# Kernel optimization log

Hardware: AMD Instinct MI355X
Metric: run time of the kernel (lower is better)

## Reference

```python
import jax, jax.numpy as jnp
import numpy as np

HIDDEN = 2048
HEADS = 16
HEAD_DIM = HIDDEN // HEADS  # 128
B, S = 2, 2048
SCALE = 1.0 / np.sqrt(HEAD_DIM)


def setup_inputs() -> dict:
    key = jax.random.key(0)
    ks = jax.random.split(key, 9)
    x = jax.random.normal(ks[0], (B, S, HIDDEN), dtype=jnp.float32)
    # causal mask, broadcastable to [B, 1(group), H, S, S]
    mask = jnp.tril(jnp.ones((S, S), dtype=bool))[None, None, None, :, :]
    mask = jnp.broadcast_to(mask, (B, 1, 1, S, S))
    s = 0.02
    Wq = jax.random.normal(ks[1], (HIDDEN, HIDDEN), dtype=jnp.float32) * s
    bq = jnp.zeros((HIDDEN,), dtype=jnp.float32)
    Wk = jax.random.normal(ks[2], (HIDDEN, HEAD_DIM), dtype=jnp.float32) * s
    bk = jnp.zeros((HEAD_DIM,), dtype=jnp.float32)
    Wv = jax.random.normal(ks[3], (HIDDEN, HEAD_DIM), dtype=jnp.float32) * s
    bv = jnp.zeros((HEAD_DIM,), dtype=jnp.float32)
    Wo = jax.random.normal(ks[4], (HIDDEN, HIDDEN), dtype=jnp.float32) * s
    bo = jnp.zeros((HIDDEN,), dtype=jnp.float32)
    return {"x": x, "mask": mask, "Wq": Wq, "bq": bq, "Wk": Wk, "bk": bk,
            "Wv": Wv, "bv": bv, "Wo": Wo, "bo": bo}


def reference(x, mask, Wq, bq, Wk, bk, Wv, bv, Wo, bo):
    b, s, _ = x.shape
    q = (x @ Wq + bq).reshape(b, s, HEADS, HEAD_DIM)   # [b,s,h,d]
    k = x @ Wk + bk                                    # [b,t,d] single shared KV head
    v = x @ Wv + bv                                    # [b,t,d]
    # scores: [b, h, s, t]; add group dim to match mask [b,1,h,s,t]
    scores = jnp.einsum('bshd,btd->bhst', q, k) * SCALE
    scores = scores[:, None]                            # [b,1,h,s,t]
    scores = jnp.where(mask, scores, jnp.float32(-jnp.inf))
    att = jax.nn.softmax(scores, axis=-1)[:, 0]         # [b,h,s,t] (dropout eval = identity)
    out = jnp.einsum('bhst,btd->bshd', att, v).reshape(b, s, HIDDEN)
    return out @ Wo + bo
```

## Files before the change

kernel.cpp:

```cpp
#include <hip/hip_runtime.h>


#define HIDDEN 2048
#define NHEADS 16
#define HDIM 128
#define BATCH 2
#define SEQ 2048
#define SCALE_L2E 0.1275258653864023f

typedef __attribute__((ext_vector_type(8))) short bfrag;
typedef __attribute__((ext_vector_type(4))) float facc;
typedef __attribute__((ext_vector_type(4))) unsigned int uifrag;

__device__ __forceinline__ unsigned short f2bf(float f) {
  unsigned int u = __float_as_uint(f);
  u += 0x7fffu + ((u >> 16) & 1u);
  return (unsigned short)(u >> 16);
}

__device__ __forceinline__ unsigned int cvt_pk_bf16(float lo, float hi) {
  unsigned int r;
  asm("v_cvt_pk_bf16_f32 %0, %1, %2" : "=v"(r) : "v"(lo), "v"(hi));
  return r;
}

__device__ __forceinline__ void gl_lds16(const void* g, void* l) {
  __builtin_amdgcn_global_load_lds(
      (const __attribute__((address_space(1))) void*)g,
      (__attribute__((address_space(3))) void*)l, 16, 0, 0);
}

#define SBAR() __builtin_amdgcn_s_barrier()
#define CFENCE() asm volatile("" ::: "memory")
#define WAIT_VM(n) asm volatile("s_waitcnt vmcnt(" #n ")" ::: "memory")

__global__ __launch_bounds__(256) void prep(const float* __restrict__ x,
                                            unsigned int* __restrict__ xb4,
                                            const float* __restrict__ Wq,
                                            const float* __restrict__ Wk,
                                            const float* __restrict__ Wv,
                                            const float* __restrict__ Wo,
                                            short* __restrict__ WqkvT,
                                            short* __restrict__ WoT, int n4) {
  if (blockIdx.z == 2) {
    int stride = gridDim.x * gridDim.y * 256;
    int i = ((int)blockIdx.y * gridDim.x + blockIdx.x) * 256 + threadIdx.x;
    for (; i < n4; i += stride) {
      float4 v = ((const float4*)x)[i];
      uint2 o = {cvt_pk_bf16(v.x, v.y), cvt_pk_bf16(v.z, v.w)};
      ((uint2*)xb4)[i] = o;
    }
    return;
  }
  const float* W;
  short* WT;
  int N;
  float s;
  int bx = blockIdx.x;
  if (blockIdx.z == 0) {
    if (bx < 64) { W = Wq; WT = WqkvT; N = HIDDEN; s = SCALE_L2E; }
    else { W = Wk; WT = WqkvT + (size_t)HIDDEN * HIDDEN; N = HDIM; s = 1.f; bx -= 64; }
  } else {
    if (bx < 64) { W = Wo; WT = WoT; N = HIDDEN; s = 1.f; }
    else { W = Wv; WT = WqkvT + (size_t)(HIDDEN + HDIM) * HIDDEN; N = HDIM; s = 1.f; bx -= 64; }
  }
  __shared__ float t[32][33];
  int tx = threadIdx.x & 31, ty = threadIdx.x >> 5;
  int n0 = bx * 32, k0 = blockIdx.y * 32;
#pragma unroll
  for (int j = 0; j < 4; ++j)
    t[ty + j * 8][tx] = W[(size_t)(k0 + ty + j * 8) * N + n0 + tx];
  __syncthreads();
#pragma unroll
  for (int j = 0; j < 4; ++j)
    WT[(size_t)(n0 + ty + j * 8) * HIDDEN + k0 + tx] = (short)f2bf(t[tx][ty + j * 8] * s);
}

__device__ __forceinline__ int pv_perm64(int row) {
  int k = row & 63;
  int p = (k & 0x23) | ((k & 0x0C) << 1) | ((k & 0x10) >> 2);
  return (row & ~63) | p;
}

__global__ __launch_bounds__(512, 6) void gemm_qkv(const short* __restrict__ A,
                                                   const short* __restrict__ BT,
                                                   const float* __restrict__ bq,
                                                   const float* __restrict__ bk,
                                                   const float* __restrict__ bv,
                                                   unsigned short* __restrict__ Qb,
                                                   unsigned short* __restrict__ Kb,
                                                   unsigned short* __restrict__ Vtb,
                                                   int M, int K) {
  __shared__ __align__(16) short Al[2][128 * 32];
  __shared__ __align__(16) short Bl[2][128 * 32];
  const int tid = threadIdx.x;
  const int w = tid >> 6, l = tid & 63;
  const int wm = w >> 1, wn = w & 1;
  const int l15 = l & 15, l4 = l >> 4;
  const int m0 = blockIdx.x * 128, n0 = blockIdx.y * 128;

  const short *ap, *bp;
  {
    int C = w * 64 + l;
    int row = C >> 2, c = C & 3;
    int sz = (c ^ (row & 3)) << 3;
    ap = A + (size_t)(m0 + row) * K + sz;
    bp = BT + (size_t)(n0 + row) * K + sz;
  }
  int aoffs[2], boffs[4];
#pragma unroll
  for (int mt = 0; mt < 2; ++mt) {
    int row = wm * 32 + mt * 16 + l15;
    aoffs[mt] = row * 64 + ((l4 ^ (row & 3)) << 4);
  }
#pragma unroll
  for (int nt = 0; nt < 4; ++nt) {
    int row = wn * 64 + nt * 16 + l15;
    boffs[nt] = row * 64 + ((l4 ^ (row & 3)) << 4);
  }

  facc acc[2][4] = {};
  const int nkt = K >> 5;
  gl_lds16(ap, &Al[0][w * 512]);
  gl_lds16(bp, &Bl[0][w * 512]);
  for (int kt = 0; kt < nkt; ++kt) {
    const int cur = kt & 1;
    if (kt + 1 < nkt) {
      gl_lds16(ap + (kt + 1) * 32, &Al[cur ^ 1][w * 512]);
      gl_lds16(bp + (kt + 1) * 32, &Bl[cur ^ 1][w * 512]);
      WAIT_VM(2);
    } else {
      WAIT_VM(0);
    }
    SBAR();
    CFENCE();
    const char* AlB = (const char*)Al + (cur << 13);
    const char* BlB = (const char*)Bl + (cur << 13);
    __builtin_amdgcn_s_setprio(1);
    bfrag af[2], bf[4];
#pragma unroll
    for (int mt = 0; mt < 2; ++mt) af[mt] = *(const bfrag*)(AlB + aoffs[mt]);
#pragma unroll
    for (int nt = 0; nt < 4; ++nt) bf[nt] = *(const bfrag*)(BlB + boffs[nt]);
#pragma unroll
    for (int mt = 0; mt < 2; ++mt)
#pragma unroll
      for (int nt = 0; nt < 4; ++nt)
        acc[mt][nt] = __builtin_amdgcn_mfma_f32_16x16x32_bf16(af[mt], bf[nt],
                                                              acc[mt][nt], 0, 0, 0);
    __builtin_amdgcn_s_setprio(0);
    CFENCE();
    SBAR();
    CFENCE();
  }
#pragma unroll
  for (int mt = 0; mt < 2; ++mt) {
#pragma unroll
    for (int nt = 0; nt < 4; ++nt) {
#pragma unroll
      for (int r = 0; r < 4; ++r) {
        int row = m0 + wm * 32 + mt * 16 + l4 * 4 + r;
        int col = n0 + wn * 64 + nt * 16 + l15;
        float v = acc[mt][nt][r];
        if (col < HIDDEN) {
          Qb[(size_t)row * HIDDEN + col] = f2bf(v + bq[col] * SCALE_L2E);
        } else if (col < HIDDEN + HDIM) {
          int lc = col - HIDDEN;
          Kb[(size_t)row * HDIM + lc] = f2bf(v + bk[lc]);
        } else {
          int lc = col - HIDDEN - HDIM;
          Vtb[(size_t)lc * M + pv_perm64(row)] = f2bf(v + bv[lc]);
        }
      }
    }
  }
}

#define GEMM_STAGE8(buf, kt)                                                   \
  _Pragma("unroll") for (int it_ = 0; it_ < 2; ++it_) {                        \
    gl_lds16(ap[it_] + (kt) * 64, &Al[buf][(w * 2 + it_) * 512]);              \
    gl_lds16(bp[it_] + (kt) * 64, &Bl[buf][(w * 2 + it_) * 512]);              \
  }

__global__ __launch_bounds__(512, 4) void gemm_out(const short* __restrict__ A,
                                                   const short* __restrict__ BT,
                                                   const float* __restrict__ bias,
                                                   float* __restrict__ Cout,
                                                   int M, int N, int K) {
  __shared__ __align__(16) short Al[2][128 * 64];
  __shared__ __align__(16) short Bl[2][128 * 64];
  const int tid = threadIdx.x;
  const int w = tid >> 6, l = tid & 63;
  const int wm = w >> 1, wn = w & 1;
  const int l15 = l & 15, l4 = l >> 4;
  const int m0 = blockIdx.x * 128, n0 = blockIdx.y * 128;
  facc acc[2][4] = {};
  const int nkt = K >> 6;
  const short *ap[2], *bp[2];
#pragma unroll
  for (int it_ = 0; it_ < 2; ++it_) {
    int C = (w * 2 + it_) * 64 + l;
    int row = C >> 3, c = C & 7;
    int sz = (c ^ (row & 7)) << 3;
    ap[it_] = A + (size_t)(m0 + row) * K + sz;
    bp[it_] = BT + (size_t)(n0 + row) * K + sz;
  }
  int aoffs[2][2], boffs[2][4];
#pragma unroll
  for (int ks = 0; ks < 2; ++ks) {
#pragma unroll
    for (int mt = 0; mt < 2; ++mt) {
      int row = wm * 32 + mt * 16 + l15, c = ks * 4 + l4;
      aoffs[ks][mt] = row * 128 + ((c ^ (row & 7)) << 4);
    }
#pragma unroll
    for (int nt = 0; nt < 4; ++nt) {
      int row = wn * 64 + nt * 16 + l15, c = ks * 4 + l4;
      boffs[ks][nt] = row * 128 + ((c ^ (row & 7)) << 4);
    }
  }
  GEMM_STAGE8(0, 0)
  for (int kt = 0; kt < nkt; ++kt) {
    const int cur = kt & 1;
    if (kt + 1 < nkt) {
      GEMM_STAGE8(cur ^ 1, kt + 1)
      WAIT_VM(4);
    } else {
      WAIT_VM(0);
    }
    SBAR();
    CFENCE();
    const char* AlB = (const char*)Al + (cur << 14);
    const char* BlB = (const char*)Bl + (cur << 14);
    __builtin_amdgcn_s_setprio(1);
#pragma unroll
    for (int ks = 0; ks < 2; ++ks) {
      bfrag af[2], bf[4];
#pragma unroll
      for (int mt = 0; mt < 2; ++mt) af[mt] = *(const bfrag*)(AlB + aoffs[ks][mt]);
#pragma unroll
      for (int nt = 0; nt < 4; ++nt) bf[nt] = *(const bfrag*)(BlB + boffs[ks][nt]);
#pragma unroll
      for (int mt = 0; mt < 2; ++mt)
#pragma unroll
        for (int nt = 0; nt < 4; ++nt)
          acc[mt][nt] = __builtin_amdgcn_mfma_f32_16x16x32_bf16(af[mt], bf[nt],
                                                                acc[mt][nt], 0, 0, 0);
    }
    __builtin_amdgcn_s_setprio(0);
    CFENCE();
    SBAR();
    CFENCE();
  }
#pragma unroll
  for (int mt = 0; mt < 2; ++mt)
#pragma unroll
    for (int nt = 0; nt < 4; ++nt)
#pragma unroll
      for (int r = 0; r < 4; ++r) {
        int row = m0 + wm * 32 + mt * 16 + l4 * 4 + r;
        int col = n0 + wn * 64 + nt * 16 + l15;
        Cout[(size_t)row * N + col] = acc[mt][nt][r] + bias[col];
      }
}

__global__ __launch_bounds__(256, 2) void attn_kernel(const short* __restrict__ Q,
                                                      const short* __restrict__ Kg,
                                                      const short* __restrict__ Vt,
                                                      unsigned short* __restrict__ O) {
  __shared__ __align__(16) short Kl[2][64 * 128];
  __shared__ __align__(16) short Vl[2][128 * 64];
  const int tid = threadIdx.x;
  const int w = tid >> 6, l = tid & 63;
  const int l15 = l & 15, l4 = l >> 4;
  const int h = blockIdx.y, b = blockIdx.z;

  int kgo[4], vgo[4];
#pragma unroll
  for (int it = 0; it < 4; ++it) {
    int C = (w * 4 + it) * 64 + l;
    int key = C >> 4, ck = C & 15;
    kgo[it] = key * HDIM + ((ck ^ (key & 7)) << 3);
    int d = C >> 3, cv = C & 7;
    vgo[it] = d * (BATCH * SEQ) + ((cv ^ (d & 7)) << 3);
  }
  int koffs[16], voffs[16];
#pragma unroll
  for (int kk = 0; kk < 4; ++kk)
#pragma unroll
    for (int kt = 0; kt < 4; ++kt) {
      int key = kt * 16 + l15, c = kk * 4 + l4;
      koffs[kk * 4 + kt] = key * 256 + ((c ^ (key & 7)) << 4);
    }
#pragma unroll
  for (int c = 0; c < 2; ++c)
#pragma unroll
    for (int nt = 0; nt < 8; ++nt) {
      int d = nt * 16 + l15, cc = c * 4 + l4;
      voffs[c * 8 + nt] = d * 128 + ((cc ^ (d & 7)) << 4);
    }
  const short* kg0 = Kg + (size_t)b * SEQ * HDIM;
  const short* vg0 = Vt + (size_t)b * SEQ;

#define STAGE_KV(buf, t)                                                       \
  do {                                                                         \
    const short* kgp = kg0 + (size_t)(t) * (64 * HDIM);                        \
    const short* vgp = vg0 + (size_t)(t) * 64;                                 \
    _Pragma("unroll") for (int it = 0; it < 4; ++it)                           \
        gl_lds16(kgp + kgo[it], &Kl[buf][(w * 4 + it) * 512]);                 \
    _Pragma("unroll") for (int it = 0; it < 4; ++it)                           \
        gl_lds16(vgp + vgo[it], &Vl[buf][(w * 4 + it) * 512]);                 \
  } while (0)

  for (int pass = 0; pass < 2; ++pass) {
    const int qtile = (pass == 0) ? (int)blockIdx.x : 31 - (int)blockIdx.x;
    const int q0 = qtile * 64;
    const int qw = q0 + w * 16;

    bfrag aq[4];
#pragma unroll
    for (int kk = 0; kk < 4; ++kk)
      aq[kk] = *(const bfrag*)(Q + (size_t)(b * SEQ + qw + l15) * HIDDEN +
                               h * HDIM + kk * 32 + l4 * 8);

    facc accO[8] = {};
    float mrow = -INFINITY, lrow = 0.f;
    const int nkv = qtile + 1;

    STAGE_KV(0, 0);

    for (int t = 0; t < nkv; ++t) {
      const int cur = t & 1;
      if (t + 1 < nkv) {
        STAGE_KV(cur ^ 1, t + 1);
        WAIT_VM(8);
      } else {
        WAIT_VM(0);
      }
      SBAR();
      CFENCE();
      const int kv0 = t << 6;
      const char* KlB = (const char*)Kl + (cur << 14);
      const char* VlB = (const char*)Vl + (cur << 14);

      facc sac[4] = {};
      __builtin_amdgcn_s_setprio(1);
#pragma unroll
      for (int kk = 0; kk < 4; ++kk) {
#pragma unroll
        for (int kt = 0; kt < 4; ++kt) {
          bfrag ak = *(const bfrag*)(KlB + koffs[kk * 4 + kt]);
          sac[kt] = __builtin_amdgcn_mfma_f32_16x16x32_bf16(ak, aq[kk], sac[kt], 0, 0, 0);
        }
      }
      __builtin_amdgcn_s_setprio(0);

      bfrag bv[16];
#pragma unroll
      for (int i = 0; i < 16; ++i)
        bv[i] = *(const bfrag*)(VlB + voffs[i]);
      CFENCE();
      SBAR();
      CFENCE();

      const int qg = qw + l15;
      const bool needmask = (kv0 + 63 > qw);
      float p[4][4];
#pragma unroll
      for (int kt = 0; kt < 4; ++kt)
#pragma unroll
        for (int r = 0; r < 4; ++r) {
          float v = sac[kt][r];
          if (needmask) {
            int keyg = kv0 + kt * 16 + l4 * 4 + r;
            v = (keyg <= qg) ? v : -INFINITY;
          }
          p[kt][r] = v;
        }
      float m0_ = fmaxf(fmaxf(p[0][0], p[0][1]), fmaxf(p[0][2], p[0][3]));
      float m1_ = fmaxf(fmaxf(p[1][0], p[1][1]), fmaxf(p[1][2], p[1][3]));
      float m2_ = fmaxf(fmaxf(p[2][0], p[2][1]), fmaxf(p[2][2], p[2][3]));
      float m3_ = fmaxf(fmaxf(p[3][0], p[3][1]), fmaxf(p[3][2], p[3][3]));
      float mt = fmaxf(fmaxf(m0_, m1_), fmaxf(m2_, m3_));
      mt = fmaxf(mt, __shfl_xor(mt, 16));
      mt = fmaxf(mt, __shfl_xor(mt, 32));
      if (!__all(mt <= mrow + 8.0f)) {
        float mn = fmaxf(mrow, mt);
        float f = exp2f(mrow - mn);
        mrow = mn;
        lrow *= f;
        float fr[4];
#pragma unroll
        for (int r = 0; r < 4; ++r) fr[r] = __shfl(f, l4 * 4 + r);
#pragma unroll
        for (int nt = 0; nt < 8; ++nt)
#pragma unroll
          for (int r = 0; r < 4; ++r) accO[nt][r] *= fr[r];
      }
#pragma unroll
      for (int kt = 0; kt < 4; ++kt)
#pragma unroll
        for (int r = 0; r < 4; ++r) p[kt][r] = exp2f(p[kt][r] - mrow);
      float s0_ = (p[0][0] + p[0][1]) + (p[0][2] + p[0][3]);
      float s1_ = (p[1][0] + p[1][1]) + (p[1][2] + p[1][3]);
      float s2_ = (p[2][0] + p[2][1]) + (p[2][2] + p[2][3]);
      float s3_ = (p[3][0] + p[3][1]) + (p[3][2] + p[3][3]);
      float ps = (s0_ + s1_) + (s2_ + s3_);
      ps += __shfl_xor(ps, 16);
      ps += __shfl_xor(ps, 32);
      lrow += ps;

      __builtin_amdgcn_s_setprio(1);
#pragma unroll
      for (int c = 0; c < 2; ++c) {
        uifrag up;
        up.x = cvt_pk_bf16(p[2 * c][0], p[2 * c][1]);
        up.y = cvt_pk_bf16(p[2 * c][2], p[2 * c][3]);
        up.z = cvt_pk_bf16(p[2 * c + 1][0], p[2 * c + 1][1]);
        up.w = cvt_pk_bf16(p[2 * c + 1][2], p[2 * c + 1][3]);
        bfrag pa = __builtin_bit_cast(bfrag, up);
#pragma unroll
        for (int nt = 0; nt < 8; ++nt)
          accO[nt] = __builtin_amdgcn_mfma_f32_16x16x32_bf16(pa, bv[c * 8 + nt],
                                                             accO[nt], 0, 0, 0);
      }
      __builtin_amdgcn_s_setprio(0);
    }

    float inv = 1.f / lrow;
#pragma unroll
    for (int r = 0; r < 4; ++r) {
      float invr = __shfl(inv, l4 * 4 + r);
      int row = qw + l4 * 4 + r;
#pragma unroll
      for (int nt = 0; nt < 8; ++nt)
        O[(size_t)(b * SEQ + row) * HIDDEN + h * HDIM + nt * 16 + l15] =
            f2bf(accO[nt][r] * invr);
    }
  }
#undef STAGE_KV
}

extern "C" void kernel_launch(void* const* d_in, const int* in_sizes, int n_in,
                              void* d_out, int out_size, void* d_ws, size_t ws_size,
                              hipStream_t stream) {
  const float* x = (const float*)d_in[0];
  const float* Wq = (const float*)d_in[2];
  const float* bq = (const float*)d_in[3];
  const float* Wk = (const float*)d_in[4];
  const float* bk = (const float*)d_in[5];
  const float* Wv = (const float*)d_in[6];
  const float* bv = (const float*)d_in[7];
  const float* Wo = (const float*)d_in[8];
  const float* bo = (const float*)d_in[9];
  float* out = (float*)d_out;

  const size_t MS = (size_t)BATCH * SEQ;
  char* ws = (char*)d_ws;
  short* xb = (short*)ws;      ws += MS * HIDDEN * 2;
  short* WqkvT = (short*)ws;   ws += (size_t)(HIDDEN + 2 * HDIM) * HIDDEN * 2;
  short* WoT = (short*)ws;     ws += (size_t)HIDDEN * HIDDEN * 2;
  short* Qb = (short*)ws;      ws += MS * HIDDEN * 2;
  short* Kb = (short*)ws;      ws += MS * HDIM * 2;
  short* Vtb = (short*)ws;     ws += (size_t)HDIM * MS * 2;
  short* Ab = (short*)ws;      ws += MS * HIDDEN * 2;

  prep<<<dim3(68, 64, 3), 256, 0, stream>>>(x, (unsigned int*)xb, Wq, Wk, Wv, Wo,
                                            WqkvT, WoT, (int)(MS * HIDDEN / 4));

  gemm_qkv<<<dim3(32, 18), 512, 0, stream>>>(xb, WqkvT, bq, bk, bv,
                                             (unsigned short*)Qb, (unsigned short*)Kb,
                                             (unsigned short*)Vtb, (int)MS, HIDDEN);

  attn_kernel<<<dim3(16, NHEADS, BATCH), 256, 0, stream>>>(Qb, Kb, Vtb,
                                                           (unsigned short*)Ab);

  gemm_out<<<dim3(32, 16), 512, 0, stream>>>(Ab, WoT, bo, out, (int)MS, HIDDEN, HIDDEN);
}
```

Measured before the change: 185.0 us.

## Process two 16-row query subtiles per wave to reuse K/V fragments

Each block now owns one 128-row query tile instead of two paired 64-row tiles processed in sequence. Each wave handles 32 query rows as two 16-row subtiles that share every K and V fragment read from LDS. This halves the K/V LDS reads and staging per query row and removes the second pass. In exchange, accumulator and softmax-state registers double, which may lower occupancy. Per-block work is no longer balanced by pairing tiles, so blocks range from 2 to 32 KV iterations.

```diff
diff --git a/kernel.cpp b/kernel.cpp
--- a/kernel.cpp
+++ b/kernel.cpp
@@ -312,65 +312,70 @@
         gl_lds16(vgp + vgo[it], &Vl[buf][(w * 4 + it) * 512]);                 \
   } while (0)
 
-  for (int pass = 0; pass < 2; ++pass) {
-    const int qtile = (pass == 0) ? (int)blockIdx.x : 31 - (int)blockIdx.x;
-    const int q0 = qtile * 64;
-    const int qw = q0 + w * 16;
-
-    bfrag aq[4];
+  const int qtile = (blockIdx.x < 8) ? (int)blockIdx.x : 23 - (int)blockIdx.x;
+  const int q0 = qtile * 128;
+  const int qw = q0 + w * 32;
+
+  bfrag aq[2][4];
+#pragma unroll
+  for (int s = 0; s < 2; ++s)
 #pragma unroll
     for (int kk = 0; kk < 4; ++kk)
-      aq[kk] = *(const bfrag*)(Q + (size_t)(b * SEQ + qw + l15) * HIDDEN +
-                               h * HDIM + kk * 32 + l4 * 8);
-
-    facc accO[8] = {};
-    float mrow = -INFINITY, lrow = 0.f;
-    const int nkv = qtile + 1;
-
-    STAGE_KV(0, 0);
-
-    for (int t = 0; t < nkv; ++t) {
-      const int cur = t & 1;
-      if (t + 1 < nkv) {
-        STAGE_KV(cur ^ 1, t + 1);
-        WAIT_VM(8);
-      } else {
-        WAIT_VM(0);
-      }
-      SBAR();
-      CFENCE();
-      const int kv0 = t << 6;
-      const char* KlB = (const char*)Kl + (cur << 14);
-      const char* VlB = (const char*)Vl + (cur << 14);
-
-      facc sac[4] = {};
-      __builtin_amdgcn_s_setprio(1);
-#pragma unroll
-      for (int kk = 0; kk < 4; ++kk) {
-#pragma unroll
-        for (int kt = 0; kt < 4; ++kt) {
-          bfrag ak = *(const bfrag*)(KlB + koffs[kk * 4 + kt]);
-          sac[kt] = __builtin_amdgcn_mfma_f32_16x16x32_bf16(ak, aq[kk], sac[kt], 0, 0, 0);
-        }
-      }
-      __builtin_amdgcn_s_setprio(0);
-
-      bfrag bv[16];
-#pragma unroll
-      for (int i = 0; i < 16; ++i)
-        bv[i] = *(const bfrag*)(VlB + voffs[i]);
-      CFENCE();
-      SBAR();
-      CFENCE();
-
-      const int qg = qw + l15;
-      const bool needmask = (kv0 + 63 > qw);
+      aq[s][kk] = *(const bfrag*)(Q + (size_t)(b * SEQ + qw + s * 16 + l15) * HIDDEN +
+                                  h * HDIM + kk * 32 + l4 * 8);
+
+  facc accO[2][8] = {};
+  float mrow[2] = {-INFINITY, -INFINITY}, lrow[2] = {0.f, 0.f};
+  const int nkv = 2 * qtile + 2;
+
+  STAGE_KV(0, 0);
+
+  for (int t = 0; t < nkv; ++t) {
+    const int cur = t & 1;
+    if (t + 1 < nkv) {
+      STAGE_KV(cur ^ 1, t + 1);
+      WAIT_VM(8);
+    } else {
+      WAIT_VM(0);
+    }
+    SBAR();
+    CFENCE();
+    const int kv0 = t << 6;
+    const char* KlB = (const char*)Kl + (cur << 14);
+    const char* VlB = (const char*)Vl + (cur << 14);
+
+    facc sac[2][4] = {};
+    __builtin_amdgcn_s_setprio(1);
+#pragma unroll
+    for (int kk = 0; kk < 4; ++kk) {
+#pragma unroll
+      for (int kt = 0; kt < 4; ++kt) {
+        bfrag ak = *(const bfrag*)(KlB + koffs[kk * 4 + kt]);
+        sac[0][kt] = __builtin_amdgcn_mfma_f32_16x16x32_bf16(ak, aq[0][kk], sac[0][kt], 0, 0, 0);
+        sac[1][kt] = __builtin_amdgcn_mfma_f32_16x16x32_bf16(ak, aq[1][kk], sac[1][kt], 0, 0, 0);
+      }
+    }
+    __builtin_amdgcn_s_setprio(0);
+
+    bfrag bv[16];
+#pragma unroll
+    for (int i = 0; i < 16; ++i)
+      bv[i] = *(const bfrag*)(VlB + voffs[i]);
+    CFENCE();
+    SBAR();
+    CFENCE();
+
+    unsigned int u[2][8];
+#pragma unroll
+    for (int s = 0; s < 2; ++s) {
+      const int qg = qw + s * 16 + l15;
+      const bool needmask = (kv0 + 63 > qw + s * 16);
       float p[4][4];
 #pragma unroll
       for (int kt = 0; kt < 4; ++kt)
 #pragma unroll
         for (int r = 0; r < 4; ++r) {
-          float v = sac[kt][r];
+          float v = sac[s][kt][r];
           if (needmask) {
             int keyg = kv0 + kt * 16 + l4 * 4 + r;
             v = (keyg <= qg) ? v : -INFINITY;
@@ -384,23 +389,23 @@
       float mt = fmaxf(fmaxf(m0_, m1_), fmaxf(m2_, m3_));
       mt = fmaxf(mt, __shfl_xor(mt, 16));
       mt = fmaxf(mt, __shfl_xor(mt, 32));
-      if (!__all(mt <= mrow + 8.0f)) {
-        float mn = fmaxf(mrow, mt);
-        float f = exp2f(mrow - mn);
-        mrow = mn;
-        lrow *= f;
+      if (!__all(mt <= mrow[s] + 8.0f)) {
+        float mn = fmaxf(mrow[s], mt);
+        float f = exp2f(mrow[s] - mn);
+        mrow[s] = mn;
+        lrow[s] *= f;
         float fr[4];
 #pragma unroll
         for (int r = 0; r < 4; ++r) fr[r] = __shfl(f, l4 * 4 + r);
 #pragma unroll
         for (int nt = 0; nt < 8; ++nt)
 #pragma unroll
-          for (int r = 0; r < 4; ++r) accO[nt][r] *= fr[r];
+          for (int r = 0; r < 4; ++r) accO[s][nt][r] *= fr[r];
       }
 #pragma unroll
       for (int kt = 0; kt < 4; ++kt)
 #pragma unroll
-        for (int r = 0; r < 4; ++r) p[kt][r] = exp2f(p[kt][r] - mrow);
+        for (int r = 0; r < 4; ++r) p[kt][r] = exp2f(p[kt][r] - mrow[s]);
       float s0_ = (p[0][0] + p[0][1]) + (p[0][2] + p[0][3]);
       float s1_ = (p[1][0] + p[1][1]) + (p[1][2] + p[1][3]);
       float s2_ = (p[2][0] + p[2][1]) + (p[2][2] + p[2][3]);
@@ -408,34 +413,45 @@
       float ps = (s0_ + s1_) + (s2_ + s3_);
       ps += __shfl_xor(ps, 16);
       ps += __shfl_xor(ps, 32);
-      lrow += ps;
-
-      __builtin_amdgcn_s_setprio(1);
-#pragma unroll
-      for (int c = 0; c < 2; ++c) {
+      lrow[s] += ps;
+#pragma unroll
+      for (int kt = 0; kt < 4; ++kt) {
+        u[s][kt * 2 + 0] = cvt_pk_bf16(p[kt][0], p[kt][1]);
+        u[s][kt * 2 + 1] = cvt_pk_bf16(p[kt][2], p[kt][3]);
+      }
+    }
+
+    __builtin_amdgcn_s_setprio(1);
+#pragma unroll
+    for (int c = 0; c < 2; ++c) {
+#pragma unroll
+      for (int s = 0; s < 2; ++s) {
         uifrag up;
-        up.x = cvt_pk_bf16(p[2 * c][0], p[2 * c][1]);
-        up.y = cvt_pk_bf16(p[2 * c][2], p[2 * c][3]);
-        up.z = cvt_pk_bf16(p[2 * c + 1][0], p[2 * c + 1][1]);
-        up.w = cvt_pk_bf16(p[2 * c + 1][2], p[2 * c + 1][3]);
+        up.x = u[s][c * 4 + 0];
+        up.y = u[s][c * 4 + 1];
+        up.z = u[s][c * 4 + 2];
+        up.w = u[s][c * 4 + 3];
         bfrag pa = __builtin_bit_cast(bfrag, up);
 #pragma unroll
         for (int nt = 0; nt < 8; ++nt)
-          accO[nt] = __builtin_amdgcn_mfma_f32_16x16x32_bf16(pa, bv[c * 8 + nt],
-                                                             accO[nt], 0, 0, 0);
-      }
-      __builtin_amdgcn_s_setprio(0);
-    }
-
-    float inv = 1.f / lrow;
+          accO[s][nt] = __builtin_amdgcn_mfma_f32_16x16x32_bf16(pa, bv[c * 8 + nt],
+                                                                accO[s][nt], 0, 0, 0);
+      }
+    }
+    __builtin_amdgcn_s_setprio(0);
+  }
+
+#pragma unroll
+  for (int s = 0; s < 2; ++s) {
+    float inv = 1.f / lrow[s];
 #pragma unroll
     for (int r = 0; r < 4; ++r) {
       float invr = __shfl(inv, l4 * 4 + r);
-      int row = qw + l4 * 4 + r;
+      int row = qw + s * 16 + l4 * 4 + r;
 #pragma unroll
       for (int nt = 0; nt < 8; ++nt)
         O[(size_t)(b * SEQ + row) * HIDDEN + h * HDIM + nt * 16 + l15] =
-            f2bf(accO[nt][r] * invr);
+            f2bf(accO[s][nt][r] * invr);
     }
   }
 #undef STAGE_KV
```

Result: slower. 222.4 us (+20.2%).
